# Optimization experiments

Measured on AMD Instinct MI355X. Metric: run time of the kernel, lower is better.

Reference implementation:

```python
import jax, jax.numpy as jnp
import numpy as np

B, D = 4096, 1024
N_CLASSES = 100
INF = jnp.float32(3.4e38)


def setup_inputs() -> dict:
    key = jax.random.key(0)
    k1, k2 = jax.random.split(key)
    x = jax.random.normal(k1, (B, 1, D), dtype=jnp.float32)
    labels = jax.random.randint(k2, (B,), 0, N_CLASSES)
    return {"x": x, "labels": labels}


def _awareness_scan(xs, labels_f, R_init):
    # xs: [B, D] float32, labels_f: [B] float32
    b, d = xs.shape
    slots = jnp.arange(b)

    def step(state, inp):
        refs, ref_labels, n_refs, count, min_d, max_d, R = state
        xi, li = inp
        mask = slots < n_refs  # active reference slots
        # distances from candidate to current reference set (torch.cdist, p=2)
        d_all = jnp.sqrt(jnp.sum((refs - xi[None, :]) ** 2, axis=-1))  # [B]
        d_all = jax.lax.stop_gradient(d_all)
        d_act = jnp.where(mask, d_all, INF)
        min_act = jnp.min(d_act)
        is_first = count == 1
        # new reference iff ALL active distances exceed R (i.e. min > R)
        insert = is_first | (min_act > R)
        refs2 = jnp.where(insert, refs.at[n_refs].set(xi), refs)
        ref_labels2 = jnp.where(insert, ref_labels.at[n_refs].set(li), ref_labels)
        n_refs2 = n_refs + insert.astype(n_refs.dtype)
        # dynamic ray update (skipped on the very first sample, as in torch)
        max_act = jnp.max(jnp.where(mask, d_all, -INF))
        min_d2 = jnp.where(is_first, min_d, jnp.minimum(min_d, min_act))
        max_d2 = jnp.where(is_first, max_d, jnp.maximum(max_d, max_act))
        R2 = jnp.where(is_first, R, (min_d2 + max_d2) / 3)
        # prediction: nearest reference AFTER potential insertion
        mask2 = slots < n_refs2
        d2 = jnp.sqrt(jnp.sum((refs2 - xi[None, :]) ** 2, axis=-1))
        d2 = jax.lax.stop_gradient(d2)
        idx = jnp.argmin(jnp.where(mask2, d2, INF))
        pred = ref_labels2[idx]
        new_state = (refs2, ref_labels2, n_refs2, count + 1, min_d2, max_d2, R2)
        return new_state, pred

    init = (
        jnp.zeros((b, d), jnp.float32),   # reference instances buffer
        jnp.zeros((b,), jnp.float32),     # reference labels buffer
        jnp.int32(0),                     # n_refs
        jnp.int32(1),                     # count (starts at 1, as in torch)
        INF,                              # min_dist
        jnp.float32(0.0),                 # max_dist
        jnp.float32(R_init),              # R
    )
    _, preds = jax.lax.scan(step, init, (xs, labels_f))
    return preds  # [B] float32


def reference(x, labels):
    # x: [B, 1, D]; labels: [B] int. update_ref_insts=True, set_labels=labels.
    xs = x.reshape(x.shape[0], x.shape[2])
    labels_f = labels.astype(jnp.float32)
    return _awareness_scan(xs, labels_f, 1.0)
```

## Files before the change

### kernel.cpp

```cpp
#include <hip/hip_runtime.h>
#include <stdint.h>

#define B_N   4096
#define D_DIM 1024
#define INF_F 3.4e38f

typedef float floatx4 __attribute__((ext_vector_type(4)));

#define XQ_OFF 131072

__global__ __launch_bounds__(256)
void k_prep(const float* __restrict__ x, unsigned char* __restrict__ xq,
            float* __restrict__ norms,
            unsigned long long* __restrict__ minpack,
            unsigned int* __restrict__ maxbits) {
    const int row = blockIdx.x;
    const int t   = threadIdx.x;
    float4 v = ((const float4*)x)[row * 256 + t];
    int p = __builtin_amdgcn_cvt_pk_fp8_f32(v.x, v.y, 0, false);
    p     = __builtin_amdgcn_cvt_pk_fp8_f32(v.z, v.w, p, true);
    const int kb = t >> 5, c = (t >> 2) & 7, r3 = row & 7;
    ((int*)xq)[(kb * 512 + (row >> 3)) * 256 + r3 * 32 + (c ^ r3) * 4 + (t & 3)] = p;
    float sq = v.x * v.x + v.y * v.y + v.z * v.z + v.w * v.w;
    #pragma unroll
    for (int off = 32; off; off >>= 1) sq += __shfl_down(sq, off);
    __shared__ float ws4[4];
    if ((t & 63) == 0) ws4[t >> 6] = sq;
    __syncthreads();
    if (t == 0) {
        norms[row]   = ws4[0] + ws4[1] + ws4[2] + ws4[3];
        minpack[row] = 0xFFFFFFFFFFFFFFFFull;
        maxbits[row] = 0u;
    }
}

#define GLDS(g, l)                                                              \
    __builtin_amdgcn_global_load_lds(                                           \
        (__attribute__((address_space(1))) void*)(void*)(g),                    \
        (__attribute__((address_space(3))) void*)(void*)(l), 16, 0, 0)

__global__ __launch_bounds__(512, 6)
void k_pass1_fp8(const unsigned char* __restrict__ xq,
                 const float* __restrict__ norms,
                 unsigned long long* __restrict__ minpack,
                 unsigned int* __restrict__ maxbits) {
    int bid = blockIdx.x;
    int ti  = (int)((sqrtf(8.f * bid + 1.f) - 1.f) * 0.5f);
    while ((ti + 1) * (ti + 2) / 2 <= bid) ti++;
    while (ti * (ti + 1) / 2 > bid) ti--;
    int tj  = bid - ti * (ti + 1) / 2;

    __shared__ unsigned char As[16384];
    __shared__ unsigned char Bs[16384];
    __shared__ unsigned long long redMin[128][2];
    __shared__ float redMax[128][2];

    const int t    = threadIdx.x;
    const int w    = t >> 6, lane = t & 63;
    const int wm   = w >> 1, wn = w & 1;
    const int q4   = lane >> 4, c15 = lane & 15;
    const int i0   = ti * 128, j0 = tj * 128;

    const unsigned char* gA[2]; const unsigned char* gB[2];
    unsigned char* lA[2]; unsigned char* lB[2];
    #pragma unroll
    for (int q = 0; q < 2; q++) {
        int e = w * 2 + q;
        gA[q] = xq + ((size_t)(i0 >> 3) + e) * 1024 + lane * 16;
        gB[q] = xq + ((size_t)(j0 >> 3) + e) * 1024 + lane * 16;
        lA[q] = As + e * 1024;
        lB[q] = Bs + e * 1024;
    }

    const int r7 = c15 & 7;
    int oib[4];
    #pragma unroll
    for (int kk = 0; kk < 4; kk++) {
        int sl  = kk * 2 + (q4 >> 1);
        oib[kk] = (((sl ^ r7) << 4) | ((q4 & 1) << 3));
    }
    int rbA[2], rbB[4];
    #pragma unroll
    for (int st = 0; st < 2; st++) rbA[st] = (wm * 32 + st * 16 + c15) * 128;
    #pragma unroll
    for (int st = 0; st < 4; st++) rbB[st] = (wn * 64 + st * 16 + c15) * 128;

    floatx4 acc[2][4];
    #pragma unroll
    for (int m = 0; m < 2; m++)
        #pragma unroll
        for (int n = 0; n < 4; n++)
            acc[m][n] = (floatx4){0.f, 0.f, 0.f, 0.f};

    for (int it = 0; it < 8; it++) {
        __syncthreads();
        #pragma unroll
        for (int q = 0; q < 2; q++) {
            GLDS(gA[q], lA[q]);
            GLDS(gB[q], lB[q]);
            gA[q] += 512 * 1024;
            gB[q] += 512 * 1024;
        }
        __syncthreads();
        #pragma unroll
        for (int kk = 0; kk < 4; kk++) {
            long long af[2], bfr[4];
            #pragma unroll
            for (int st = 0; st < 2; st++)
                af[st]  = *(const long long*)(As + rbA[st] + oib[kk]);
            #pragma unroll
            for (int st = 0; st < 4; st++)
                bfr[st] = *(const long long*)(Bs + rbB[st] + oib[kk]);
            #pragma unroll
            for (int m = 0; m < 2; m++)
                #pragma unroll
                for (int n = 0; n < 4; n++)
                    acc[m][n] = __builtin_amdgcn_mfma_f32_16x16x32_fp8_fp8(
                        af[m], bfr[n], acc[m][n], 0, 0, 0);
        }
    }

    float nj[4];
    #pragma unroll
    for (int st = 0; st < 4; st++) nj[st] = norms[j0 + wn * 64 + st * 16 + c15];

    #pragma unroll
    for (int st_m = 0; st_m < 2; st_m++) {
        #pragma unroll
        for (int r = 0; r < 4; r++) {
            int i_loc = wm * 32 + st_m * 16 + q4 * 4 + r;
            int gi    = i0 + i_loc;
            float ni  = norms[gi];
            unsigned long long mp = 0xFFFFFFFFFFFFFFFFull;
            float mx = -INF_F;
            #pragma unroll
            for (int st_n = 0; st_n < 4; st_n++) {
                int gj = j0 + wn * 64 + st_n * 16 + c15;
                if (gj < gi) {
                    float dot = acc[st_m][st_n][r];
                    float d2  = fmaxf(ni + nj[st_n] - 2.f * dot, 0.f);
                    unsigned long long p =
                        ((unsigned long long)__float_as_uint(d2) << 32) | (unsigned)gj;
                    if (p < mp) mp = p;
                    mx = fmaxf(mx, d2);
                }
            }
            #pragma unroll
            for (int off = 1; off < 16; off <<= 1) {
                unsigned long long op = __shfl_xor(mp, off, 64);
                if (op < mp) mp = op;
                float om = __shfl_xor(mx, off, 64);
                mx = fmaxf(mx, om);
            }
            if (c15 == 0) { redMin[i_loc][wn] = mp; redMax[i_loc][wn] = mx; }
        }
    }
    __syncthreads();
    if (t < 128) {
        unsigned long long mp = redMin[t][0];
        if (redMin[t][1] < mp) mp = redMin[t][1];
        float mx = fmaxf(redMax[t][0], redMax[t][1]);
        if (mp != 0xFFFFFFFFFFFFFFFFull) {
            atomicMin(&minpack[i0 + t], mp);
            atomicMax(&maxbits[i0 + t], __float_as_uint(mx));
        }
    }
}

__global__ __launch_bounds__(1024)
void k_tail(const unsigned long long* __restrict__ minpack,
            const unsigned int* __restrict__ maxbits,
            const float* __restrict__ x, const float* __restrict__ norms,
            const int* __restrict__ labels, int* __restrict__ ref_idx,
            float* __restrict__ out) {
    const int t    = threadIdx.x;
    const int lane = t & 63, wid = t >> 6;
    float m[4], M[4];
    #pragma unroll
    for (int q = 0; q < 4; q++) {
        int i = t * 4 + q;
        unsigned long long p = minpack[i];
        float dmin = (p == 0xFFFFFFFFFFFFFFFFull)
                       ? INF_F : sqrtf(__uint_as_float((unsigned)(p >> 32)));
        m[q] = (i == 0) ? INF_F : dmin;
        M[q] = (i == 0) ? -INF_F : sqrtf(__uint_as_float(maxbits[i]));
    }
    float pmin[4], pmax[4];
    pmin[0] = m[0]; pmax[0] = M[0];
    #pragma unroll
    for (int q = 1; q < 4; q++) {
        pmin[q] = fminf(pmin[q - 1], m[q]);
        pmax[q] = fmaxf(pmax[q - 1], M[q]);
    }
    float wmin = pmin[3], wmax = pmax[3];
    #pragma unroll
    for (int off = 1; off < 64; off <<= 1) {
        float a = __shfl_up(wmin, off, 64);
        float b = __shfl_up(wmax, off, 64);
        if (lane >= off) { wmin = fminf(wmin, a); wmax = fmaxf(wmax, b); }
    }
    __shared__ float swmin[16], swmax[16];
    if (lane == 63) { swmin[wid] = wmin; swmax[wid] = wmax; }
    __syncthreads();
    float exwMin = INF_F, exwMax = -INF_F;
    for (int k = 0; k < wid; k++) {
        exwMin = fminf(exwMin, swmin[k]);
        exwMax = fmaxf(exwMax, swmax[k]);
    }
    float upMin = __shfl_up(wmin, 1, 64);
    float upMax = __shfl_up(wmax, 1, 64);
    float exMin = fminf(exwMin, (lane > 0) ? upMin : INF_F);
    float exMax = fmaxf(exwMax, (lane > 0) ? upMax : -INF_F);

    int viol = B_N;
    #pragma unroll
    for (int q = 0; q < 4; q++) {
        int i = t * 4 + q;
        if (i >= 1) {
            float pm = (q == 0) ? exMin : fminf(exMin, pmin[q - 1]);
            float pM = (q == 0) ? exMax : fmaxf(exMax, pmax[q - 1]);
            float R  = (i == 1) ? 1.0f : (pm + pM) / 3.0f;
            if (!(m[q] > R) && i < viol) viol = i;
        }
    }
    int vw = viol;
    #pragma unroll
    for (int off = 32; off; off >>= 1) vw = min(vw, __shfl_down(vw, off, 64));
    __shared__ int svw[16];
    if (lane == 0) svw[wid] = vw;
    __syncthreads();
    int s_star = B_N;
    for (int k = 0; k < 16; k++) s_star = min(s_star, svw[k]);

    for (int i = t; i < s_star; i += 1024) out[i] = (float)labels[i];

    __shared__ float s_state[3];
    __shared__ int s_n;
    if (s_star < B_N && t == (s_star >> 2)) {
        int q = s_star & 3;
        float pm = (q == 0) ? exMin : fminf(exMin, pmin[q - 1]);
        float pM = (q == 0) ? exMax : fmaxf(exMax, pmax[q - 1]);
        float md = fminf(pm, m[q]);
        float Md = fmaxf(pM, M[q]);
        s_state[0] = md; s_state[1] = Md; s_state[2] = (md + Md) / 3.0f;
        s_n = s_star;
        unsigned long long p = minpack[s_star];
        int j = (int)(unsigned)(p & 0xFFFFFFFFu);
        out[s_star] = (float)labels[j];
    }
    if (s_star >= B_N) return;

    for (int s = t; s < s_star; s += 1024) ref_idx[s] = s;
    __syncthreads();

    __shared__ unsigned long long redp[1024];
    __shared__ float redm[1024];
    for (int i = s_star + 1; i < B_N; i++) {
        int n = s_n;
        const float* xi = x + (size_t)i * D_DIM;
        float ni = norms[i];
        unsigned long long mp = 0xFFFFFFFFFFFFFFFFull;
        float mx = -INF_F;
        for (int slot = t; slot < n; slot += 1024) {
            int j = ref_idx[slot];
            const float* xj = x + (size_t)j * D_DIM;
            float dot = 0.f;
            for (int k = 0; k < D_DIM; k++) dot = fmaf(xi[k], xj[k], dot);
            float d = sqrtf(fmaxf(ni + norms[j] - 2.f * dot, 0.f));
            unsigned long long p =
                ((unsigned long long)__float_as_uint(d) << 32) | (unsigned)slot;
            if (p < mp) mp = p;
            mx = fmaxf(mx, d);
        }
        redp[t] = mp; redm[t] = mx;
        __syncthreads();
        for (int off = 512; off; off >>= 1) {
            if (t < off) {
                if (redp[t + off] < redp[t]) redp[t] = redp[t + off];
                redm[t] = fmaxf(redm[t], redm[t + off]);
            }
            __syncthreads();
        }
        if (t == 0) {
            unsigned long long p = redp[0];
            float min_act = __uint_as_float((unsigned)(p >> 32));
            int minslot   = (int)(unsigned)(p & 0xFFFFFFFFu);
            float max_act = redm[0];
            bool insert = (min_act > s_state[2]);
            int pred;
            if (insert) {
                ref_idx[n] = i;
                s_n = n + 1;
                pred = (min_act <= 0.0f) ? labels[ref_idx[minslot]] : labels[i];
            } else {
                pred = labels[ref_idx[minslot]];
            }
            float md = fminf(s_state[0], min_act);
            float Md = fmaxf(s_state[1], max_act);
            s_state[0] = md; s_state[1] = Md; s_state[2] = (md + Md) / 3.0f;
            out[i] = (float)pred;
        }
        __syncthreads();
    }
}

extern "C" void kernel_launch(void* const* d_in, const int* in_sizes, int n_in,
                              void* d_out, int out_size, void* d_ws, size_t ws_size,
                              hipStream_t stream) {
    const float* x      = (const float*)d_in[0];
    const int*   labels = (const int*)d_in[1];
    float*       out    = (float*)d_out;
    char* ws = (char*)d_ws;
    unsigned long long* minpack = (unsigned long long*)ws;
    unsigned int*       maxbits = (unsigned int*)(ws + 32768);
    float*              norms   = (float*)(ws + 49152);
    int*                ref_idx = (int*)(ws + 65600);
    unsigned char*      xq      = (unsigned char*)(ws + XQ_OFF);

    k_prep<<<B_N, 256, 0, stream>>>(x, xq, norms, minpack, maxbits);
    const int ntiles  = B_N / 128;
    const int nblocks = ntiles * (ntiles + 1) / 2;
    k_pass1_fp8<<<nblocks, 512, 0, stream>>>(xq, norms, minpack, maxbits);
    k_tail<<<1, 1024, 0, stream>>>(minpack, maxbits, x, norms, labels, ref_idx, out);
}
```

Measured before the change: 99.32 us.

## Load A operand directly from global in MFMA fragment layout, drop A LDS

The prep kernel now writes a second FP8 copy of the inputs laid out so each lane can load its MFMA A-fragments straight from global memory with 16-byte loads. Shared memory staging of A is removed and the warp grid changes from 4x2 to 2x4, so each wave computes 64x32 instead of 32x64, and the reduction buffers widen to four columns. B fragments are read as 16-byte LDS loads once per k-block. This aims to cut LDS traffic and footprint, at the cost of extra global loads, a second quantized buffer and a lower occupancy hint in launch bounds.

```diff
diff --git a/kernel.cpp b/kernel.cpp
--- a/kernel.cpp
+++ b/kernel.cpp
@@ -6,12 +6,14 @@
 #define INF_F 3.4e38f
 
 typedef float floatx4 __attribute__((ext_vector_type(4)));
-
-#define XQ_OFF 131072
+typedef long long llx2 __attribute__((ext_vector_type(2)));
+
+#define XQB_OFF 131072
+#define XQA_OFF 4325376
 
 __global__ __launch_bounds__(256)
-void k_prep(const float* __restrict__ x, unsigned char* __restrict__ xq,
-            float* __restrict__ norms,
+void k_prep(const float* __restrict__ x, unsigned char* __restrict__ xqB,
+            unsigned char* __restrict__ xqA, float* __restrict__ norms,
             unsigned long long* __restrict__ minpack,
             unsigned int* __restrict__ maxbits) {
     const int row = blockIdx.x;
@@ -19,8 +21,16 @@
     float4 v = ((const float4*)x)[row * 256 + t];
     int p = __builtin_amdgcn_cvt_pk_fp8_f32(v.x, v.y, 0, false);
     p     = __builtin_amdgcn_cvt_pk_fp8_f32(v.z, v.w, p, true);
-    const int kb = t >> 5, c = (t >> 2) & 7, r3 = row & 7;
-    ((int*)xq)[(kb * 512 + (row >> 3)) * 256 + r3 * 32 + (c ^ r3) * 4 + (t & 3)] = p;
+    const int it  = t >> 5;
+    const int kk  = (t >> 3) & 3;
+    const int kk2 = kk >> 1;
+    const int q4  = (t >> 1) & 3;
+    const int lo2 = (kk & 1) * 2 + (t & 1);
+    const int r3  = row & 7;
+    ((int*)xqB)[(it * 512 + (row >> 3)) * 256 + r3 * 32 +
+                (((kk2 * 4 + q4) ^ r3) * 4) + lo2] = p;
+    ((int*)xqA)[(((it * 128 + (row >> 5)) * 2 + ((row >> 4) & 1)) * 2 + kk2) * 256 +
+                (q4 * 16 + (row & 15)) * 4 + lo2] = p;
     float sq = v.x * v.x + v.y * v.y + v.z * v.z + v.w * v.w;
     #pragma unroll
     for (int off = 32; off; off >>= 1) sq += __shfl_down(sq, off);
@@ -39,8 +49,9 @@
         (__attribute__((address_space(1))) void*)(void*)(g),                    \
         (__attribute__((address_space(3))) void*)(void*)(l), 16, 0, 0)
 
-__global__ __launch_bounds__(512, 6)
-void k_pass1_fp8(const unsigned char* __restrict__ xq,
+__global__ __launch_bounds__(512, 4)
+void k_pass1_fp8(const unsigned char* __restrict__ xqB,
+                 const unsigned char* __restrict__ xqA,
                  const float* __restrict__ norms,
                  unsigned long long* __restrict__ minpack,
                  unsigned int* __restrict__ maxbits) {
@@ -50,95 +61,96 @@
     while (ti * (ti + 1) / 2 > bid) ti--;
     int tj  = bid - ti * (ti + 1) / 2;
 
-    __shared__ unsigned char As[16384];
     __shared__ unsigned char Bs[16384];
-    __shared__ unsigned long long redMin[128][2];
-    __shared__ float redMax[128][2];
+    __shared__ unsigned long long redMin[128][4];
+    __shared__ float redMax[128][4];
 
     const int t    = threadIdx.x;
     const int w    = t >> 6, lane = t & 63;
-    const int wm   = w >> 1, wn = w & 1;
+    const int wm   = w >> 2, wn = w & 3;
     const int q4   = lane >> 4, c15 = lane & 15;
+    const int r7   = c15 & 7;
     const int i0   = ti * 128, j0 = tj * 128;
 
-    const unsigned char* gA[2]; const unsigned char* gB[2];
-    unsigned char* lA[2]; unsigned char* lB[2];
+    const unsigned char* gB[2]; unsigned char* lB[2];
     #pragma unroll
     for (int q = 0; q < 2; q++) {
         int e = w * 2 + q;
-        gA[q] = xq + ((size_t)(i0 >> 3) + e) * 1024 + lane * 16;
-        gB[q] = xq + ((size_t)(j0 >> 3) + e) * 1024 + lane * 16;
-        lA[q] = As + e * 1024;
+        gB[q] = xqB + ((size_t)(j0 >> 3) + e) * 1024 + lane * 16;
         lB[q] = Bs + e * 1024;
     }
-
-    const int r7 = c15 & 7;
-    int oib[4];
-    #pragma unroll
-    for (int kk = 0; kk < 4; kk++) {
-        int sl  = kk * 2 + (q4 >> 1);
-        oib[kk] = (((sl ^ r7) << 4) | ((q4 & 1) << 3));
-    }
-    int rbA[2], rbB[4];
-    #pragma unroll
-    for (int st = 0; st < 2; st++) rbA[st] = (wm * 32 + st * 16 + c15) * 128;
-    #pragma unroll
-    for (int st = 0; st < 4; st++) rbB[st] = (wn * 64 + st * 16 + c15) * 128;
-
-    floatx4 acc[2][4];
-    #pragma unroll
-    for (int m = 0; m < 2; m++)
-        #pragma unroll
-        for (int n = 0; n < 4; n++)
+    const unsigned char* gA[4][2];
+    #pragma unroll
+    for (int st = 0; st < 4; st++)
+        #pragma unroll
+        for (int kk2 = 0; kk2 < 2; kk2++)
+            gA[st][kk2] = xqA +
+                ((size_t)((((i0 >> 5) + wm * 2 + (st >> 1)) * 2 + (st & 1)) * 2 + kk2))
+                    * 1024 + lane * 16;
+    int rbB[2][2];
+    #pragma unroll
+    for (int sn = 0; sn < 2; sn++)
+        #pragma unroll
+        for (int kk2 = 0; kk2 < 2; kk2++)
+            rbB[sn][kk2] = (wn * 32 + sn * 16 + c15) * 128 +
+                           (((kk2 * 4 + q4) ^ r7) << 4);
+
+    floatx4 acc[4][2];
+    #pragma unroll
+    for (int m = 0; m < 4; m++)
+        #pragma unroll
+        for (int n = 0; n < 2; n++)
             acc[m][n] = (floatx4){0.f, 0.f, 0.f, 0.f};
 
     for (int it = 0; it < 8; it++) {
         __syncthreads();
-        #pragma unroll
-        for (int q = 0; q < 2; q++) {
-            GLDS(gA[q], lA[q]);
-            GLDS(gB[q], lB[q]);
-            gA[q] += 512 * 1024;
-            gB[q] += 512 * 1024;
-        }
+        GLDS(gB[0], lB[0]); GLDS(gB[1], lB[1]);
+        gB[0] += 512 * 1024; gB[1] += 512 * 1024;
+        llx2 aq[4][2];
+        #pragma unroll
+        for (int st = 0; st < 4; st++)
+            #pragma unroll
+            for (int kk2 = 0; kk2 < 2; kk2++) {
+                aq[st][kk2] = *(const llx2*)(gA[st][kk2]);
+                gA[st][kk2] += 512 * 1024;
+            }
         __syncthreads();
-        #pragma unroll
-        for (int kk = 0; kk < 4; kk++) {
-            long long af[2], bfr[4];
-            #pragma unroll
-            for (int st = 0; st < 2; st++)
-                af[st]  = *(const long long*)(As + rbA[st] + oib[kk]);
-            #pragma unroll
-            for (int st = 0; st < 4; st++)
-                bfr[st] = *(const long long*)(Bs + rbB[st] + oib[kk]);
-            #pragma unroll
-            for (int m = 0; m < 2; m++)
+        llx2 bq[2][2];
+        #pragma unroll
+        for (int sn = 0; sn < 2; sn++)
+            #pragma unroll
+            for (int kk2 = 0; kk2 < 2; kk2++)
+                bq[sn][kk2] = *(const llx2*)(Bs + rbB[sn][kk2]);
+        #pragma unroll
+        for (int kk = 0; kk < 4; kk++)
+            #pragma unroll
+            for (int m = 0; m < 4; m++)
                 #pragma unroll
-                for (int n = 0; n < 4; n++)
+                for (int n = 0; n < 2; n++)
                     acc[m][n] = __builtin_amdgcn_mfma_f32_16x16x32_fp8_fp8(
-                        af[m], bfr[n], acc[m][n], 0, 0, 0);
-        }
-    }
-
-    float nj[4];
-    #pragma unroll
-    for (int st = 0; st < 4; st++) nj[st] = norms[j0 + wn * 64 + st * 16 + c15];
-
-    #pragma unroll
-    for (int st_m = 0; st_m < 2; st_m++) {
+                        aq[m][kk >> 1][kk & 1], bq[n][kk >> 1][kk & 1],
+                        acc[m][n], 0, 0, 0);
+    }
+
+    float nj[2];
+    #pragma unroll
+    for (int sn = 0; sn < 2; sn++) nj[sn] = norms[j0 + wn * 32 + sn * 16 + c15];
+
+    #pragma unroll
+    for (int st_m = 0; st_m < 4; st_m++) {
         #pragma unroll
         for (int r = 0; r < 4; r++) {
-            int i_loc = wm * 32 + st_m * 16 + q4 * 4 + r;
+            int i_loc = wm * 64 + st_m * 16 + q4 * 4 + r;
             int gi    = i0 + i_loc;
             float ni  = norms[gi];
             unsigned long long mp = 0xFFFFFFFFFFFFFFFFull;
             float mx = -INF_F;
             #pragma unroll
-            for (int st_n = 0; st_n < 4; st_n++) {
-                int gj = j0 + wn * 64 + st_n * 16 + c15;
+            for (int sn = 0; sn < 2; sn++) {
+                int gj = j0 + wn * 32 + sn * 16 + c15;
                 if (gj < gi) {
-                    float dot = acc[st_m][st_n][r];
-                    float d2  = fmaxf(ni + nj[st_n] - 2.f * dot, 0.f);
+                    float dot = acc[st_m][sn][r];
+                    float d2  = fmaxf(ni + nj[sn] - 2.f * dot, 0.f);
                     unsigned long long p =
                         ((unsigned long long)__float_as_uint(d2) << 32) | (unsigned)gj;
                     if (p < mp) mp = p;
@@ -158,8 +170,12 @@
     __syncthreads();
     if (t < 128) {
         unsigned long long mp = redMin[t][0];
-        if (redMin[t][1] < mp) mp = redMin[t][1];
-        float mx = fmaxf(redMax[t][0], redMax[t][1]);
+        float mx = redMax[t][0];
+        #pragma unroll
+        for (int c = 1; c < 4; c++) {
+            if (redMin[t][c] < mp) mp = redMin[t][c];
+            mx = fmaxf(mx, redMax[t][c]);
+        }
         if (mp != 0xFFFFFFFFFFFFFFFFull) {
             atomicMin(&minpack[i0 + t], mp);
             atomicMax(&maxbits[i0 + t], __float_as_uint(mx));
@@ -315,11 +331,12 @@
     unsigned int*       maxbits = (unsigned int*)(ws + 32768);
     float*              norms   = (float*)(ws + 49152);
     int*                ref_idx = (int*)(ws + 65600);
-    unsigned char*      xq      = (unsigned char*)(ws + XQ_OFF);
-
-    k_prep<<<B_N, 256, 0, stream>>>(x, xq, norms, minpack, maxbits);
+    unsigned char*      xqB     = (unsigned char*)(ws + XQB_OFF);
+    unsigned char*      xqA     = (unsigned char*)(ws + XQA_OFF);
+
+    k_prep<<<B_N, 256, 0, stream>>>(x, xqB, xqA, norms, minpack, maxbits);
     const int ntiles  = B_N / 128;
     const int nblocks = ntiles * (ntiles + 1) / 2;
-    k_pass1_fp8<<<nblocks, 512, 0, stream>>>(xq, norms, minpack, maxbits);
+    k_pass1_fp8<<<nblocks, 512, 0, stream>>>(xqB, xqA, norms, minpack, maxbits);
     k_tail<<<1, 1024, 0, stream>>>(minpack, maxbits, x, norms, labels, ref_idx, out);
 }
```

Measured after the change: 110.4 us. 1.11x slower.
